# Optimization experiments

Measured on AMD Instinct MI355X. Metric: run time of the kernel, lower is better.

The kernel has to match this reference:

```python
import jax, jax.numpy as jnp
from jax import lax
import numpy as np
import math

T, B, F = 512, 256, 256  # num_steps, batch, input_size == hidden_size
H = F


def setup_inputs() -> dict:
    key = jax.random.key(0)
    ks = jax.random.split(key, 20)
    stdv = 1.0 / math.sqrt(H)

    def u(k, n):
        return jax.random.uniform(k, (n,), jnp.float32, -stdv, stdv)

    X = jax.random.normal(ks[0], (T, B, F), jnp.float32)
    Mask = (jax.random.uniform(ks[1], (T, B, F)) < 0.7).astype(jnp.float32)
    Delta = jax.random.uniform(ks[2], (T, B, F), jnp.float32)

    return {
        "X": X, "Mask": Mask, "Delta": Delta,
        "x_mean": u(ks[3], F),
        "w_dg_x": u(ks[4], F), "b_dg_x": u(ks[5], F),
        "w_dg_h": u(ks[6], H), "b_dg_h": u(ks[7], H),
        "w_xz": u(ks[8], F), "u_hz": u(ks[9], H), "b_z": u(ks[10], H),
        "w_xr": u(ks[11], F), "u_hr": u(ks[12], H), "b_r": u(ks[13], H),
        "w_xh": u(ks[14], F), "u_hh": u(ks[15], H), "v_mh": u(ks[16], F),
        "b_h": u(ks[17], H),
    }


def reference(X, Mask, Delta, x_mean, w_dg_x, b_dg_x, w_dg_h, b_dg_h,
              w_xz, u_hz, b_z, w_xr, u_hr, b_r, w_xh, u_hh, v_mh, b_h):
    batch = X.shape[1]

    def step(h, inp):
        x, m, d = inp  # each [B, F]
        gamma_x = jnp.exp(-jnp.maximum(0.0, w_dg_x * d + b_dg_x))
        gamma_h = jnp.exp(-jnp.maximum(0.0, w_dg_h * d + b_dg_h))
        x = m * x + (1.0 - m) * (gamma_x * x + (1.0 - gamma_x) * x_mean)
        h = gamma_h * h
        z = jax.nn.sigmoid(w_xz * x + u_hz * h + b_z)
        r = jax.nn.sigmoid(w_xr * x + u_hr * h + b_r)
        h_tilde = jnp.tanh(w_xh * x + u_hh * (r * h) + v_mh * m + b_h)
        h = (1.0 - z) * h + z * h_tilde
        return h, h

    h0 = jnp.zeros((batch, H), X.dtype)
    _, hs = lax.scan(step, h0, (X, Mask, Delta))  # hs: [T, B, H]
    hidden_states = jnp.transpose(hs, (1, 0, 2))  # [B, T, H]
    return hidden_states, hidden_states[:, -1, :]
```

## Files before the change

### kernel.cpp

```cpp
#include <hip/hip_runtime.h>
#include <math.h>


#define TT 512
#define BB 256
#define FF 256
#define PF_D 8

__device__ __forceinline__ float fast_sigmoid(float x) {
    return __builtin_amdgcn_rcpf(1.0f + __expf(-x));
}
__device__ __forceinline__ float fast_tanh(float x) {
    return fmaf(-2.0f, __builtin_amdgcn_rcpf(1.0f + __expf(2.0f * x)), 1.0f);
}

__global__ __launch_bounds__(256) void grud_kernel(
    const float* __restrict__ X, const float* __restrict__ Mask,
    const float* __restrict__ Delta,
    const float* __restrict__ x_mean,
    const float* __restrict__ w_dg_x, const float* __restrict__ b_dg_x,
    const float* __restrict__ w_dg_h, const float* __restrict__ b_dg_h,
    const float* __restrict__ w_xz, const float* __restrict__ u_hz,
    const float* __restrict__ b_z,
    const float* __restrict__ w_xr, const float* __restrict__ u_hr,
    const float* __restrict__ b_r,
    const float* __restrict__ w_xh, const float* __restrict__ u_hh,
    const float* __restrict__ v_mh, const float* __restrict__ b_h,
    float* __restrict__ out)
{
    const int g = blockIdx.x * blockDim.x + threadIdx.x;
    const int f = g & (FF - 1);
    const int b = g >> 8;

    const float xm  = x_mean[f];
    const float wdx = w_dg_x[f], bdx = b_dg_x[f];
    const float wdh = w_dg_h[f], bdh = b_dg_h[f];
    const float wxz = w_xz[f],   uhz = u_hz[f], bz = b_z[f];
    const float wxr = w_xr[f],   uhr = u_hr[f], br = b_r[f];
    const float wxh = w_xh[f],   uhh = u_hh[f];
    const float vmh = v_mh[f],   bh  = b_h[f];

    const float* xp = X     + g;
    const float* mp = Mask  + g;
    const float* dp = Delta + g;
    float* op = out + (size_t)b * (TT * FF) + f;

    float px[PF_D], pm[PF_D], pd[PF_D];
    #pragma unroll
    for (int i = 0; i < PF_D; ++i) {
        px[i] = xp[i * (BB * FF)];
        pm[i] = mp[i * (BB * FF)];
        pd[i] = dp[i * (BB * FF)];
    }

    float h = 0.0f;

    #pragma unroll PF_D
    for (int t = 0; t < TT - PF_D; ++t) {
        const int slot = t & (PF_D - 1);
        float x = px[slot], m = pm[slot], d = pd[slot];
        const int tn = t + PF_D;
        px[slot] = xp[tn * (BB * FF)];
        pm[slot] = mp[tn * (BB * FF)];
        pd[slot] = dp[tn * (BB * FF)];

        float gx = __expf(-fmaxf(0.0f, fmaf(wdx, d, bdx)));
        float gh = __expf(-fmaxf(0.0f, fmaf(wdh, d, bdh)));
        float xhat = fmaf(gx, x, (1.0f - gx) * xm);
        x = fmaf(m, x, (1.0f - m) * xhat);
        h = gh * h;
        float z  = fast_sigmoid(fmaf(wxz, x, fmaf(uhz, h, bz)));
        float r  = fast_sigmoid(fmaf(wxr, x, fmaf(uhr, h, br)));
        float ht = fast_tanh(fmaf(wxh, x, fmaf(uhh, r * h, fmaf(vmh, m, bh))));
        h = fmaf(z, ht - h, h);
        op[t * FF] = h;
    }

    #pragma unroll
    for (int t = TT - PF_D; t < TT; ++t) {
        const int slot = t & (PF_D - 1);
        float x = px[slot], m = pm[slot], d = pd[slot];

        float gx = __expf(-fmaxf(0.0f, fmaf(wdx, d, bdx)));
        float gh = __expf(-fmaxf(0.0f, fmaf(wdh, d, bdh)));
        float xhat = fmaf(gx, x, (1.0f - gx) * xm);
        x = fmaf(m, x, (1.0f - m) * xhat);
        h = gh * h;
        float z  = fast_sigmoid(fmaf(wxz, x, fmaf(uhz, h, bz)));
        float r  = fast_sigmoid(fmaf(wxr, x, fmaf(uhr, h, br)));
        float ht = fast_tanh(fmaf(wxh, x, fmaf(uhh, r * h, fmaf(vmh, m, bh))));
        h = fmaf(z, ht - h, h);
        op[t * FF] = h;
    }

    out[(size_t)BB * TT * FF + g] = h;
}

extern "C" void kernel_launch(void* const* d_in, const int* in_sizes, int n_in,
                              void* d_out, int out_size, void* d_ws, size_t ws_size,
                              hipStream_t stream) {
    const float* X      = (const float*)d_in[0];
    const float* Mask   = (const float*)d_in[1];
    const float* Delta  = (const float*)d_in[2];
    const float* x_mean = (const float*)d_in[3];
    const float* w_dg_x = (const float*)d_in[4];
    const float* b_dg_x = (const float*)d_in[5];
    const float* w_dg_h = (const float*)d_in[6];
    const float* b_dg_h = (const float*)d_in[7];
    const float* w_xz   = (const float*)d_in[8];
    const float* u_hz   = (const float*)d_in[9];
    const float* b_z    = (const float*)d_in[10];
    const float* w_xr   = (const float*)d_in[11];
    const float* u_hr   = (const float*)d_in[12];
    const float* b_r    = (const float*)d_in[13];
    const float* w_xh   = (const float*)d_in[14];
    const float* u_hh   = (const float*)d_in[15];
    const float* v_mh   = (const float*)d_in[16];
    const float* b_h    = (const float*)d_in[17];
    float* out = (float*)d_out;

    const int threads = BB * FF;
    grud_kernel<<<threads / 256, 256, 0, stream>>>(
        X, Mask, Delta, x_mean, w_dg_x, b_dg_x, w_dg_h, b_dg_h,
        w_xz, u_hz, b_z, w_xr, u_hr, b_r, w_xh, u_hh, v_mh, b_h, out);
}
```

Before: 421.5 us.

## Warp-specialize GRU-D kernel with producer threads double-buffering inputs through LDS

Splits each block into 256 producer threads that load X/Mask/Delta chunks of 8 timesteps as float4 into a double-buffered shared-memory ring, and 256 consumer threads that run the elementwise recurrence from LDS. This replaces per-thread register prefetch of scalar loads with vectorized bulk loads meant to hide global-memory latency. It adds a block-wide barrier per chunk and halves the compute threads per block, and the LDS footprint (48KB) limits occupancy.

Result: no change. 417.6 us (-0.9%).

```diff
diff --git a/kernel.cpp b/kernel.cpp
--- a/kernel.cpp
+++ b/kernel.cpp
@@ -5,7 +5,9 @@
 #define TT 512
 #define BB 256
 #define FF 256
-#define PF_D 8
+#define BF (BB * FF)
+#define CH 8
+#define NCH (TT / CH)
 
 __device__ __forceinline__ float fast_sigmoid(float x) {
     return __builtin_amdgcn_rcpf(1.0f + __expf(-x));
@@ -14,7 +16,7 @@
     return fmaf(-2.0f, __builtin_amdgcn_rcpf(1.0f + __expf(2.0f * x)), 1.0f);
 }
 
-__global__ __launch_bounds__(256) void grud_kernel(
+__global__ __launch_bounds__(512) void grud_kernel(
     const float* __restrict__ X, const float* __restrict__ Mask,
     const float* __restrict__ Delta,
     const float* __restrict__ x_mean,
@@ -28,72 +30,90 @@
     const float* __restrict__ v_mh, const float* __restrict__ b_h,
     float* __restrict__ out)
 {
-    const int g = blockIdx.x * blockDim.x + threadIdx.x;
-    const int f = g & (FF - 1);
-    const int b = g >> 8;
+    __shared__ float lds[2][3][CH][FF];
 
-    const float xm  = x_mean[f];
-    const float wdx = w_dg_x[f], bdx = b_dg_x[f];
-    const float wdh = w_dg_h[f], bdh = b_dg_h[f];
-    const float wxz = w_xz[f],   uhz = u_hz[f], bz = b_z[f];
-    const float wxr = w_xr[f],   uhr = u_hr[f], br = b_r[f];
-    const float wxh = w_xh[f],   uhh = u_hh[f];
-    const float vmh = v_mh[f],   bh  = b_h[f];
+    const int tid = threadIdx.x;
+    const int blk = blockIdx.x;
 
-    const float* xp = X     + g;
-    const float* mp = Mask  + g;
-    const float* dp = Delta + g;
-    float* op = out + (size_t)b * (TT * FF) + f;
+    if (tid >= 256) {
+        const int j = tid - 256;
+        const float* srcs[3] = { X     + (size_t)blk * FF,
+                                 Mask  + (size_t)blk * FF,
+                                 Delta + (size_t)blk * FF };
 
-    float px[PF_D], pm[PF_D], pd[PF_D];
-    #pragma unroll
-    for (int i = 0; i < PF_D; ++i) {
-        px[i] = xp[i * (BB * FF)];
-        pm[i] = mp[i * (BB * FF)];
-        pd[i] = dp[i * (BB * FF)];
+        {
+            #pragma unroll
+            for (int arr = 0; arr < 3; ++arr) {
+                const float* s = srcs[arr];
+                #pragma unroll
+                for (int i2 = 0; i2 < 2; ++i2) {
+                    const int rem  = i2 * 256 + j;
+                    const int step = rem >> 6;
+                    const int f4   = (rem & 63) << 2;
+                    *(float4*)&lds[0][arr][step][f4] =
+                        *(const float4*)(s + (size_t)step * BF + f4);
+                }
+            }
+        }
+        __syncthreads();
+
+        for (int k = 0; k < NCH; ++k) {
+            if (k + 1 < NCH) {
+                const int bufi = (k + 1) & 1;
+                const int t0   = (k + 1) * CH;
+                #pragma unroll
+                for (int arr = 0; arr < 3; ++arr) {
+                    const float* s = srcs[arr];
+                    #pragma unroll
+                    for (int i2 = 0; i2 < 2; ++i2) {
+                        const int rem  = i2 * 256 + j;
+                        const int step = rem >> 6;
+                        const int f4   = (rem & 63) << 2;
+                        *(float4*)&lds[bufi][arr][step][f4] =
+                            *(const float4*)(s + (size_t)(t0 + step) * BF + f4);
+                    }
+                }
+            }
+            __syncthreads();
+        }
+    } else {
+        const int f = tid;
+        const float xm  = x_mean[f];
+        const float wdx = w_dg_x[f], bdx = b_dg_x[f];
+        const float wdh = w_dg_h[f], bdh = b_dg_h[f];
+        const float wxz = w_xz[f],   uhz = u_hz[f], bz = b_z[f];
+        const float wxr = w_xr[f],   uhr = u_hr[f], br = b_r[f];
+        const float wxh = w_xh[f],   uhh = u_hh[f];
+        const float vmh = v_mh[f],   bh  = b_h[f];
+
+        float h = 0.0f;
+        __syncthreads();
+
+        for (int k = 0; k < NCH; ++k) {
+            const int cb = k & 1;
+            float* op = out + ((size_t)blk * TT + (size_t)k * CH) * FF + f;
+            #pragma unroll
+            for (int s = 0; s < CH; ++s) {
+                float x = lds[cb][0][s][f];
+                float m = lds[cb][1][s][f];
+                float d = lds[cb][2][s][f];
+
+                float gx = __expf(-fmaxf(0.0f, fmaf(wdx, d, bdx)));
+                float gh = __expf(-fmaxf(0.0f, fmaf(wdh, d, bdh)));
+                float xhat = fmaf(gx, x, (1.0f - gx) * xm);
+                x = fmaf(m, x, (1.0f - m) * xhat);
+                h = gh * h;
+                float z  = fast_sigmoid(fmaf(wxz, x, fmaf(uhz, h, bz)));
+                float r  = fast_sigmoid(fmaf(wxr, x, fmaf(uhr, h, br)));
+                float ht = fast_tanh(fmaf(wxh, x, fmaf(uhh, r * h, fmaf(vmh, m, bh))));
+                h = fmaf(z, ht - h, h);
+                op[s * FF] = h;
+            }
+            __syncthreads();
+        }
+
+        out[(size_t)BB * TT * FF + (size_t)blk * FF + f] = h;
     }
-
-    float h = 0.0f;
-
-    #pragma unroll PF_D
-    for (int t = 0; t < TT - PF_D; ++t) {
-        const int slot = t & (PF_D - 1);
-        float x = px[slot], m = pm[slot], d = pd[slot];
-        const int tn = t + PF_D;
-        px[slot] = xp[tn * (BB * FF)];
-        pm[slot] = mp[tn * (BB * FF)];
-        pd[slot] = dp[tn * (BB * FF)];
-
-        float gx = __expf(-fmaxf(0.0f, fmaf(wdx, d, bdx)));
-        float gh = __expf(-fmaxf(0.0f, fmaf(wdh, d, bdh)));
-        float xhat = fmaf(gx, x, (1.0f - gx) * xm);
-        x = fmaf(m, x, (1.0f - m) * xhat);
-        h = gh * h;
-        float z  = fast_sigmoid(fmaf(wxz, x, fmaf(uhz, h, bz)));
-        float r  = fast_sigmoid(fmaf(wxr, x, fmaf(uhr, h, br)));
-        float ht = fast_tanh(fmaf(wxh, x, fmaf(uhh, r * h, fmaf(vmh, m, bh))));
-        h = fmaf(z, ht - h, h);
-        op[t * FF] = h;
-    }
-
-    #pragma unroll
-    for (int t = TT - PF_D; t < TT; ++t) {
-        const int slot = t & (PF_D - 1);
-        float x = px[slot], m = pm[slot], d = pd[slot];
-
-        float gx = __expf(-fmaxf(0.0f, fmaf(wdx, d, bdx)));
-        float gh = __expf(-fmaxf(0.0f, fmaf(wdh, d, bdh)));
-        float xhat = fmaf(gx, x, (1.0f - gx) * xm);
-        x = fmaf(m, x, (1.0f - m) * xhat);
-        h = gh * h;
-        float z  = fast_sigmoid(fmaf(wxz, x, fmaf(uhz, h, bz)));
-        float r  = fast_sigmoid(fmaf(wxr, x, fmaf(uhr, h, br)));
-        float ht = fast_tanh(fmaf(wxh, x, fmaf(uhh, r * h, fmaf(vmh, m, bh))));
-        h = fmaf(z, ht - h, h);
-        op[t * FF] = h;
-    }
-
-    out[(size_t)BB * TT * FF + g] = h;
 }
 
 extern "C" void kernel_launch(void* const* d_in, const int* in_sizes, int n_in,
@@ -119,8 +139,7 @@
     const float* b_h    = (const float*)d_in[17];
     float* out = (float*)d_out;
 
-    const int threads = BB * FF;
-    grud_kernel<<<threads / 256, 256, 0, stream>>>(
+    grud_kernel<<<BB, 512, 0, stream>>>(
         X, Mask, Delta, x_mean, w_dg_x, b_dg_x, w_dg_h, b_dg_h,
         w_xz, u_hz, b_z, w_xr, u_hr, b_r, w_xh, u_hh, v_mh, b_h, out);
 }
```
